# Optimization experiments

Hardware: AMD Instinct MI355X
Metric: run time of the kernel (lower is better)

## Reference

```python
import jax, jax.numpy as jnp
import numpy as np
from jax import lax

BN_EPS = 1e-5


def _spatial_gate(x, w, g, b, m, v):
    # x: [N, C, H, W]; ChannelPool -> [N, 2, H, W]; 7x7 conv -> [N,1,H,W]; BN (eval); sigmoid gate
    comp = jnp.stack([jnp.max(x, axis=1), jnp.mean(x, axis=1)], axis=1)
    o = lax.conv_general_dilated(comp, w, (1, 1), [(3, 3), (3, 3)],
                                 dimension_numbers=('NCHW', 'OIHW', 'NCHW'))
    o = (o - m[None, :, None, None]) * lax.rsqrt(v + BN_EPS)[None, :, None, None] \
        * g[None, :, None, None] + b[None, :, None, None]
    s = jax.nn.sigmoid(o)
    return x * s


def _eca_sort(x, w_eca):
    # global avg pool -> sort channels desc -> 1D conv over sorted seq -> sigmoid -> unsort -> gate
    y = jnp.mean(x, axis=(2, 3))               # [N, C]
    order = jnp.argsort(-y, axis=1)            # descending sort indices
    rank = jnp.argsort(order, axis=1)          # inverse permutation
    ys = jnp.take_along_axis(y, order, axis=1)  # sorted descending
    k = w_eca.shape[-1]
    p = k // 2
    o = lax.conv_general_dilated(ys[:, None, :], w_eca, (1,), [(p, p)],
                                 dimension_numbers=('NCH', 'OIH', 'NCH'))[:, 0, :]
    sig = jax.nn.sigmoid(o)
    yr = jnp.take_along_axis(sig, rank, axis=1)  # reorder back per original index_select(rank)
    return x * yr[:, :, None, None]


def setup_inputs() -> dict:
    key = jax.random.key(0)
    ks = jax.random.split(key, 6)
    N, C, H, W = 32, 256, 56, 56
    inp = {
        'x': jax.random.normal(ks[0], (N, C, H, W), dtype=jnp.float32),
        'weight': jax.random.normal(ks[1], (1,), dtype=jnp.float32),
        'w_h': jax.random.normal(ks[2], (1, 2, 7, 7), dtype=jnp.float32) * 0.1,
        'g_h': jnp.ones((1,), jnp.float32), 'b_h': jnp.zeros((1,), jnp.float32),
        'm_h': jnp.zeros((1,), jnp.float32), 'v_h': jnp.ones((1,), jnp.float32),
        'w_w': jax.random.normal(ks[3], (1, 2, 7, 7), dtype=jnp.float32) * 0.1,
        'g_w': jnp.ones((1,), jnp.float32), 'b_w': jnp.zeros((1,), jnp.float32),
        'm_w': jnp.zeros((1,), jnp.float32), 'v_w': jnp.ones((1,), jnp.float32),
        'w_s': jax.random.normal(ks[4], (1, 2, 7, 7), dtype=jnp.float32) * 0.1,
        'g_s': jnp.ones((1,), jnp.float32), 'b_s': jnp.zeros((1,), jnp.float32),
        'm_s': jnp.zeros((1,), jnp.float32), 'v_s': jnp.ones((1,), jnp.float32),
        'w_eca': jax.random.normal(ks[5], (1, 1, 5), dtype=jnp.float32) * 0.3,
    }
    return inp


def reference(x, weight, w_h, g_h, b_h, m_h, v_h, w_w, g_w, b_w, m_w, v_w,
              w_s, g_s, b_s, m_s, v_s, w_eca):
    # branch 1: gate over H-as-channel (permute 0,2,1,3)
    xh = jnp.transpose(x, (0, 2, 1, 3))
    x11 = jnp.transpose(_spatial_gate(xh, w_h, g_h, b_h, m_h, v_h), (0, 2, 1, 3))
    # branch 2: gate over W-as-channel (permute 0,3,2,1)
    xw = jnp.transpose(x, (0, 3, 2, 1))
    x21 = jnp.transpose(_spatial_gate(xw, w_w, g_w, b_w, m_w, v_w), (0, 3, 2, 1))
    # branch 3: eca with sort/unsort
    x31 = _eca_sort(x, w_eca)
    # branch 4: plain spatial gate
    xo = _spatial_gate(x, w_s, g_s, b_s, m_s, v_s)
    return 0.23779 * xo + 0.24695 * x11 + 0.24365 * x21 + 0.27173 * x31
```

## Files before the change

kernel.cpp:

```cpp
#include <hip/hip_runtime.h>
#include <math.h>

#define N_ 32
#define C_ 256
#define H_ 56
#define W_ 56
#define HW_ (H_*W_)
#define HW4_ (HW_/4)
#define CHW_ (C_*HW_)
#define NHW_ (N_*HW_)
#define NHW4_ (NHW_/4)
#define NCW_ (N_*C_*W_)
#define NHC_ (N_*H_*C_)
#define BN_EPS_ 1e-5f

#define TLD 60
#define PPB 8
#define NB_PL 1024

#define SM_BUF(i) ((i) * 3360)
#define SM_YS 6720
#define SM_TOT (6720 + 8)

#define F4MAX(a,b) do { (a).x=fmaxf((a).x,(b).x); (a).y=fmaxf((a).y,(b).y); \
                        (a).z=fmaxf((a).z,(b).z); (a).w=fmaxf((a).w,(b).w); } while(0)
#define F4ADD(a,b) do { (a).x+=(b).x; (a).y+=(b).y; (a).z+=(b).z; (a).w+=(b).w; } while(0)

__global__ __launch_bounds__(256, 4) void pools_k(
        const float* __restrict__ x,
        float* __restrict__ maxH, float* __restrict__ meanH,
        float* __restrict__ maxWt, float* __restrict__ meanWt,
        float* __restrict__ pmx, float* __restrict__ psm,
        float* __restrict__ y) {
    __shared__ float smem[SM_TOT];
    int b = blockIdx.x;
    int tid = threadIdx.x;
    const float4* x4 = (const float4*)x;
    int pb0 = b * PPB;
    int row0 = tid / 14,          col0 = (tid % 14) * 4;
    int row1 = (tid + 256) / 14,  col1 = ((tid + 256) % 14) * 4;
    int row2 = (tid + 512) / 14,  col2 = ((tid + 512) % 14) * 4;
    int row3 = (tid + 768) / 14,  col3 = ((tid + 768) % 14) * 4;
    int wq = tid >> 2, q4 = tid & 3;
    bool act = tid < 224;
    int wvid = tid >> 6;
    float4 a0, a1, a2, a3, b0_, b1_, b2_, b3_;
    float4 amx0, amx1, amx2, amx3, asm0, asm1, asm2, asm3;
    amx0 = amx1 = amx2 = amx3 = make_float4(-INFINITY, -INFINITY, -INFINITY, -INFINITY);
    asm0 = asm1 = asm2 = asm3 = make_float4(0.f, 0.f, 0.f, 0.f);

#define ISSUE(R0,R1,R2,R3, P) { size_t _ba = (size_t)(pb0 + (P)) * HW4_;          \
        R0 = x4[_ba + tid]; R1 = x4[_ba + 256 + tid]; R2 = x4[_ba + 512 + tid];   \
        if (tid < 16) R3 = x4[_ba + 768 + tid]; }
#define FOLD(R0,R1,R2,R3) { F4MAX(amx0,R0); F4ADD(asm0,R0);                       \
        F4MAX(amx1,R1); F4ADD(asm1,R1); F4MAX(amx2,R2); F4ADD(asm2,R2);           \
        if (tid < 16) { F4MAX(amx3,R3); F4ADD(asm3,R3); } }
#define STAGE(BUF, R0,R1,R2,R3) { float* _d = smem + (BUF);                       \
        *(float4*)&_d[row0*TLD+col0] = R0; *(float4*)&_d[row1*TLD+col1] = R1;     \
        *(float4*)&_d[row2*TLD+col2] = R2;                                        \
        if (tid < 16) *(float4*)&_d[row3*TLD+col3] = R3; }

    ISSUE(a0, a1, a2, a3, 0);
    FOLD(a0, a1, a2, a3);
    STAGE(SM_BUF(0), a0, a1, a2, a3);
    ISSUE(b0_, b1_, b2_, b3_, 1);
    __syncthreads();

    #pragma unroll
    for (int k = 0; k < PPB; ++k) {
        if (k + 2 < PPB) {
            if ((k & 1) == 0) { ISSUE(a0, a1, a2, a3, k + 2); }
            else              { ISSUE(b0_, b1_, b2_, b3_, k + 2); }
        }
        const float* cur = smem + SM_BUF(k & 1);
        int pb = pb0 + k;
        int n = pb >> 8, c = pb & 255;
        float cmx = -INFINITY, csm = 0.f, rmx = -INFINITY, rsm = 0.f;
        if (act) {
            const float* cb = &cur[(q4 * 14) * TLD + wq];
            #pragma unroll
            for (int hh = 0; hh < 14; ++hh) {
                float v = cb[hh * TLD];
                cmx = fmaxf(cmx, v); csm += v;
            }
            const float* rb = &cur[wq * TLD + q4 * 14];
            #pragma unroll
            for (int kk = 0; kk < 14; ++kk) {
                float v = rb[kk];
                rmx = fmaxf(rmx, v); rsm += v;
            }
        }
        cmx = fmaxf(cmx, __shfl_xor(cmx, 1)); csm += __shfl_xor(csm, 1);
        cmx = fmaxf(cmx, __shfl_xor(cmx, 2)); csm += __shfl_xor(csm, 2);
        rmx = fmaxf(rmx, __shfl_xor(rmx, 1)); rsm += __shfl_xor(rsm, 1);
        rmx = fmaxf(rmx, __shfl_xor(rmx, 2)); rsm += __shfl_xor(rsm, 2);
        if (act && q4 == 0) {
            int oH = (n * C_ + c) * W_ + wq;
            maxH[oH] = cmx; meanH[oH] = csm * (1.f / H_);
            int oW = (n * C_ + c) * H_ + wq;
            maxWt[oW] = rmx; meanWt[oW] = rsm * (1.f / W_);
        }
        float rs = (act && q4 == 0) ? rsm : 0.f;
        #pragma unroll
        for (int off = 32; off >= 1; off >>= 1) rs += __shfl_xor(rs, off);
        if ((tid & 63) == 0) smem[SM_YS + (k & 1) * 4 + wvid] = rs;
        if (k > 0 && tid == 0) {
            int s = ((k - 1) & 1) * 4;
            float t = smem[SM_YS + s] + smem[SM_YS + s + 1] +
                      smem[SM_YS + s + 2] + smem[SM_YS + s + 3];
            y[pb - 1] = t * (1.f / HW_);
        }
        if (k + 1 < PPB) {
            if ((k & 1) == 0) { FOLD(b0_, b1_, b2_, b3_);
                                STAGE(SM_BUF((k + 1) & 1), b0_, b1_, b2_, b3_); }
            else              { FOLD(a0, a1, a2, a3);
                                STAGE(SM_BUF((k + 1) & 1), a0, a1, a2, a3); }
        }
        __syncthreads();
    }
    if (tid == 0) {
        int s = ((PPB - 1) & 1) * 4;
        float t = smem[SM_YS + s] + smem[SM_YS + s + 1] +
                  smem[SM_YS + s + 2] + smem[SM_YS + s + 3];
        y[pb0 + PPB - 1] = t * (1.f / HW_);
    }
#undef ISSUE
#undef FOLD
#undef STAGE
    {
        float4* PM = (float4*)pmx + (size_t)b * HW4_;
        float4* PS = (float4*)psm + (size_t)b * HW4_;
        PM[tid] = amx0;        PS[tid] = asm0;
        PM[tid + 256] = amx1;  PS[tid + 256] = asm1;
        PM[tid + 512] = amx2;  PS[tid + 512] = asm2;
        if (tid < 16) { PM[tid + 768] = amx3; PS[tid + 768] = asm3; }
    }
}

__global__ __launch_bounds__(256, 4) void cpool_final_k(
        const float* __restrict__ pmx, const float* __restrict__ psm,
        float* __restrict__ maxC, float* __restrict__ meanC) {
    __shared__ float4 smx[4][64];
    __shared__ float4 ssm[4][64];
    int bb = blockIdx.x;
    int tid = threadIdx.x;
    int oi = tid & 63, g4 = tid >> 6;
    int t = bb * 64 + oi;
    int n = t / HW4_, hw4 = t - n * HW4_;
    const float4* PM = (const float4*)pmx + (size_t)(n * 32 + g4 * 8) * HW4_ + hw4;
    const float4* PS = (const float4*)psm + (size_t)(n * 32 + g4 * 8) * HW4_ + hw4;
    float4 mx = make_float4(-INFINITY, -INFINITY, -INFINITY, -INFINITY);
    float4 sm = make_float4(0.f, 0.f, 0.f, 0.f);
    #pragma unroll
    for (int g = 0; g < 8; ++g) {
        float4 v = PM[(size_t)g * HW4_];
        float4 s = PS[(size_t)g * HW4_];
        F4MAX(mx, v);
        F4ADD(sm, s);
    }
    smx[g4][oi] = mx;
    ssm[g4][oi] = sm;
    __syncthreads();
    if (tid < 64) {
        float4 m = smx[0][tid];
        #pragma unroll
        for (int j = 1; j < 4; ++j) F4MAX(m, smx[j][tid]);
        ((float4*)maxC)[bb * 64 + tid] = m;
    } else if (tid < 128) {
        int t2 = tid - 64;
        float4 s = ssm[0][t2];
        #pragma unroll
        for (int j = 1; j < 4; ++j) F4ADD(s, ssm[j][t2]);
        s.x *= (1.f / C_); s.y *= (1.f / C_); s.z *= (1.f / C_); s.w *= (1.f / C_);
        ((float4*)meanC)[bb * 64 + t2] = s;
    }
}

template <int R, int Cc, bool TR>
__device__ __forceinline__ void conv7_part(int t, const float* __restrict__ p0,
                                           const float* __restrict__ p1,
                                           const float* __restrict__ wt,
                                           float g, float bb, float m, float v,
                                           float* __restrict__ out) {
    const int per = R * Cc;
    int n = t / per;
    int r2 = t - n * per;
    int i = r2 / Cc, j = r2 - i * Cc;
    const float* b0 = p0 + (size_t)n * per;
    const float* b1 = p1 + (size_t)n * per;
    float acc = 0.f;
    #pragma unroll
    for (int ki = 0; ki < 7; ++ki) {
        int ii = i + ki - 3;
        if (ii < 0 || ii >= R) continue;
        #pragma unroll
        for (int kj = 0; kj < 7; ++kj) {
            int jj = j + kj - 3;
            if (jj < 0 || jj >= Cc) continue;
            int idx = ii * Cc + jj;
            int wi = TR ? (kj * 7 + ki) : (ki * 7 + kj);
            acc += b0[idx] * wt[wi] + b1[idx] * wt[49 + wi];
        }
    }
    float o = (acc - m) * rsqrtf(v + BN_EPS_) * g + bb;
    out[t] = 1.f / (1.f + expf(-o));
}

#define NB_SS (NHW_ / 256)
#define NB_SH (NCW_ / 256)
#define NB_SW (NHC_ / 256)

__global__ __launch_bounds__(256) void conv_eca_k(
        const float* __restrict__ maxC, const float* __restrict__ meanC,
        const float* __restrict__ maxH, const float* __restrict__ meanH,
        const float* __restrict__ maxWt, const float* __restrict__ meanWt,
        const float* __restrict__ w_s, const float* __restrict__ g_s,
        const float* __restrict__ b_s, const float* __restrict__ m_s,
        const float* __restrict__ v_s,
        const float* __restrict__ w_h, const float* __restrict__ g_h,
        const float* __restrict__ b_h, const float* __restrict__ m_h,
        const float* __restrict__ v_h,
        const float* __restrict__ w_w, const float* __restrict__ g_w,
        const float* __restrict__ b_w, const float* __restrict__ m_w,
        const float* __restrict__ v_w,
        const float* __restrict__ y, const float* __restrict__ w_eca,
        float* __restrict__ s_s, float* __restrict__ s_h, float* __restrict__ s_wt,
        float* __restrict__ gate) {
    __shared__ float sv[C_];
    __shared__ int si[C_];
    int b = blockIdx.x;
    int tid = threadIdx.x;
    if (b < NB_SS) {
        conv7_part<H_, W_, false>(b * 256 + tid, maxC, meanC, w_s, g_s[0], b_s[0],
                                  m_s[0], v_s[0], s_s);
    } else if (b < NB_SS + NB_SH) {
        conv7_part<C_, W_, false>((b - NB_SS) * 256 + tid, maxH, meanH, w_h, g_h[0],
                                  b_h[0], m_h[0], v_h[0], s_h);
    } else if (b < NB_SS + NB_SH + NB_SW) {
        conv7_part<C_, H_, true>((b - NB_SS - NB_SH) * 256 + tid, maxWt, meanWt, w_w,
                                 g_w[0], b_w[0], m_w[0], v_w[0], s_wt);
    } else {
        int n = b - (NB_SS + NB_SH + NB_SW);
        sv[tid] = y[n * C_ + tid];
        si[tid] = tid;
        __syncthreads();
        for (int k = 2; k <= C_; k <<= 1) {
            for (int j = k >> 1; j > 0; j >>= 1) {
                int ixj = tid ^ j;
                if (ixj > tid) {
                    float v1 = sv[tid], v2 = sv[ixj];
                    int i1 = si[tid], i2 = si[ixj];
                    bool before = (v1 > v2) || (v1 == v2 && i1 < i2);
                    bool dir = ((tid & k) == 0);
                    if (dir ? !before : before) {
                        sv[tid] = v2; sv[ixj] = v1;
                        si[tid] = i2; si[ixj] = i1;
                    }
                }
                __syncthreads();
            }
        }
        float o = 0.f;
        #pragma unroll
        for (int j = 0; j < 5; ++j) {
            int p = tid + j - 2;
            if (p >= 0 && p < C_) o += sv[p] * w_eca[j];
        }
        gate[n * C_ + si[tid]] = 1.f / (1.f + expf(-o));
    }
}

__global__ __launch_bounds__(256) void apply_k(
        const float* __restrict__ x, const float* __restrict__ s_s,
        const float* __restrict__ s_h, const float* __restrict__ s_wt,
        const float* __restrict__ gate, float* __restrict__ out) {
    int t0 = blockIdx.x * 512 + threadIdx.x;
    #pragma unroll
    for (int r = 0; r < 2; ++r) {
        int t = t0 + r * 256;
        int f = t * 4;
        int n = f / CHW_;
        int rem = f - n * CHW_;
        int c = rem / HW_;
        int hw = rem - c * HW_;
        int h = hw / W_;
        int w = hw - h * W_;
        float4 xv = ((const float4*)x)[t];
        float4 s4 = *(const float4*)(s_s + (size_t)n * HW_ + hw);
        float4 h4 = *(const float4*)(s_h + ((size_t)n * C_ + c) * W_ + w);
        float sw = s_wt[((size_t)n * C_ + c) * H_ + h];
        float ge = gate[n * C_ + c];
        float base = 0.24365f * sw + 0.27173f * ge;
        float4 o;
        o.x = xv.x * (0.23779f * s4.x + 0.24695f * h4.x + base);
        o.y = xv.y * (0.23779f * s4.y + 0.24695f * h4.y + base);
        o.z = xv.z * (0.23779f * s4.z + 0.24695f * h4.z + base);
        o.w = xv.w * (0.23779f * s4.w + 0.24695f * h4.w + base);
        ((float4*)out)[t] = o;
    }
}

extern "C" void kernel_launch(void* const* d_in, const int* in_sizes, int n_in,
                              void* d_out, int out_size, void* d_ws, size_t ws_size,
                              hipStream_t stream) {
    const float* x     = (const float*)d_in[0];
    const float* w_h   = (const float*)d_in[2];
    const float* g_h   = (const float*)d_in[3];
    const float* b_h   = (const float*)d_in[4];
    const float* m_h   = (const float*)d_in[5];
    const float* v_h   = (const float*)d_in[6];
    const float* w_w   = (const float*)d_in[7];
    const float* g_w   = (const float*)d_in[8];
    const float* b_w   = (const float*)d_in[9];
    const float* m_w   = (const float*)d_in[10];
    const float* v_w   = (const float*)d_in[11];
    const float* w_s   = (const float*)d_in[12];
    const float* g_s   = (const float*)d_in[13];
    const float* b_s   = (const float*)d_in[14];
    const float* m_s   = (const float*)d_in[15];
    const float* v_s   = (const float*)d_in[16];
    const float* w_eca = (const float*)d_in[17];
    float* out = (float*)d_out;

    float* ws    = (float*)d_ws;
    float* maxC  = ws;
    float* meanC = maxC  + NHW_;
    float* maxH  = meanC + NHW_;
    float* meanH = maxH  + NCW_;
    float* maxWt = meanH + NCW_;
    float* meanWt= maxWt + NHC_;
    float* s_s   = meanWt+ NHC_;
    float* s_h   = s_s   + NHW_;
    float* s_wt  = s_h   + NCW_;
    float* yv    = s_wt  + NHC_;
    float* gate  = yv    + N_ * C_;
    float* pmx   = gate  + N_ * C_;
    float* psm   = pmx   + (size_t)NB_PL * HW_;

    pools_k<<<NB_PL, 256, 0, stream>>>(x, maxH, meanH, maxWt, meanWt, pmx, psm, yv);

    cpool_final_k<<<NHW4_ / 64, 256, 0, stream>>>(pmx, psm, maxC, meanC);

    int conv_blocks = NB_SS + NB_SH + NB_SW + N_;
    conv_eca_k<<<conv_blocks, 256, 0, stream>>>(maxC, meanC, maxH, meanH, maxWt, meanWt,
                                                w_s, g_s, b_s, m_s, v_s,
                                                w_h, g_h, b_h, m_h, v_h,
                                                w_w, g_w, b_w, m_w, v_w,
                                                yv, w_eca, s_s, s_h, s_wt, gate);

    apply_k<<<(N_ * CHW_ / 4) / 512, 256, 0, stream>>>(x, s_s, s_h, s_wt, gate, out);
}
```

Measured before the change: 112.1 us.

## Restructure pooling kernel to one wavefront per block with register-held planes

Rewrites pools_k so each 64-thread block (one wavefront) processes 8 channel planes. Each lane holds a whole column strip of the plane in registers and double-buffers two planes, in place of a 256-thread block staging tiles through shared memory with block-wide barriers. Column reductions happen in registers, and row reductions go through a small shared scratch within the wavefront, which removes __syncthreads. The trade-off is much higher register pressure (about 56 float4 registers per lane), lower occupancy, and 8 idle lanes out of 64 on the loads.

```diff
diff --git a/kernel.cpp b/kernel.cpp
--- a/kernel.cpp
+++ b/kernel.cpp
@@ -14,126 +14,108 @@
 #define NHC_ (N_*H_*C_)
 #define BN_EPS_ 1e-5f
 
-#define TLD 60
-#define PPB 8
+#define PPW 8
 #define NB_PL 1024
-
-#define SM_BUF(i) ((i) * 3360)
-#define SM_YS 6720
-#define SM_TOT (6720 + 8)
 
 #define F4MAX(a,b) do { (a).x=fmaxf((a).x,(b).x); (a).y=fmaxf((a).y,(b).y); \
                         (a).z=fmaxf((a).z,(b).z); (a).w=fmaxf((a).w,(b).w); } while(0)
 #define F4ADD(a,b) do { (a).x+=(b).x; (a).y+=(b).y; (a).z+=(b).z; (a).w+=(b).w; } while(0)
 
-__global__ __launch_bounds__(256, 4) void pools_k(
+__global__ __launch_bounds__(64) void pools_k(
         const float* __restrict__ x,
         float* __restrict__ maxH, float* __restrict__ meanH,
         float* __restrict__ maxWt, float* __restrict__ meanWt,
         float* __restrict__ pmx, float* __restrict__ psm,
         float* __restrict__ y) {
-    __shared__ float smem[SM_TOT];
-    int b = blockIdx.x;
-    int tid = threadIdx.x;
+    __shared__ float2 rowscr[56 * 15];
+    __shared__ float4 colmx[56];
+    __shared__ float4 colsm[56];
+    const int wid = blockIdx.x;
+    const int lane = threadIdx.x;
+    const int n = wid >> 5;
+    const int pb0 = wid * PPW;
     const float4* x4 = (const float4*)x;
-    int pb0 = b * PPB;
-    int row0 = tid / 14,          col0 = (tid % 14) * 4;
-    int row1 = (tid + 256) / 14,  col1 = ((tid + 256) % 14) * 4;
-    int row2 = (tid + 512) / 14,  col2 = ((tid + 512) % 14) * 4;
-    int row3 = (tid + 768) / 14,  col3 = ((tid + 768) % 14) * 4;
-    int wq = tid >> 2, q4 = tid & 3;
-    bool act = tid < 224;
-    int wvid = tid >> 6;
-    float4 a0, a1, a2, a3, b0_, b1_, b2_, b3_;
-    float4 amx0, amx1, amx2, amx3, asm0, asm1, asm2, asm3;
-    amx0 = amx1 = amx2 = amx3 = make_float4(-INFINITY, -INFINITY, -INFINITY, -INFINITY);
-    asm0 = asm1 = asm2 = asm3 = make_float4(0.f, 0.f, 0.f, 0.f);
-
-#define ISSUE(R0,R1,R2,R3, P) { size_t _ba = (size_t)(pb0 + (P)) * HW4_;          \
-        R0 = x4[_ba + tid]; R1 = x4[_ba + 256 + tid]; R2 = x4[_ba + 512 + tid];   \
-        if (tid < 16) R3 = x4[_ba + 768 + tid]; }
-#define FOLD(R0,R1,R2,R3) { F4MAX(amx0,R0); F4ADD(asm0,R0);                       \
-        F4MAX(amx1,R1); F4ADD(asm1,R1); F4MAX(amx2,R2); F4ADD(asm2,R2);           \
-        if (tid < 16) { F4MAX(amx3,R3); F4ADD(asm3,R3); } }
-#define STAGE(BUF, R0,R1,R2,R3) { float* _d = smem + (BUF);                       \
-        *(float4*)&_d[row0*TLD+col0] = R0; *(float4*)&_d[row1*TLD+col1] = R1;     \
-        *(float4*)&_d[row2*TLD+col2] = R2;                                        \
-        if (tid < 16) *(float4*)&_d[row3*TLD+col3] = R3; }
-
-    ISSUE(a0, a1, a2, a3, 0);
-    FOLD(a0, a1, a2, a3);
-    STAGE(SM_BUF(0), a0, a1, a2, a3);
-    ISSUE(b0_, b1_, b2_, b3_, 1);
-    __syncthreads();
-
-    #pragma unroll
-    for (int k = 0; k < PPB; ++k) {
-        if (k + 2 < PPB) {
-            if ((k & 1) == 0) { ISSUE(a0, a1, a2, a3, k + 2); }
-            else              { ISSUE(b0_, b1_, b2_, b3_, k + 2); }
+    const int lc = (lane < 56) ? lane : 55;
+    const int g = lane / 14;
+    const int q = lane - g * 14;
+
+    float4 A[14], B[14];
+    float4 amx[14], asum[14];
+    #pragma unroll
+    for (int t = 0; t < 14; ++t) {
+        amx[t] = make_float4(-INFINITY, -INFINITY, -INFINITY, -INFINITY);
+        asum[t] = make_float4(0.f, 0.f, 0.f, 0.f);
+    }
+
+#define ISSUE(S, P) do { size_t _ba = (size_t)(pb0 + (P)) * HW4_;                  \
+        _Pragma("unroll")                                                          \
+        for (int _t = 0; _t < 14; ++_t) S[_t] = x4[_ba + 56 * _t + lc]; } while(0)
+
+#define PLANE(S, K) do {                                                           \
+        const int _pb = pb0 + (K);                                                 \
+        const int _c = _pb & 255;                                                  \
+        float4 cmx = S[0], csm = S[0];                                             \
+        _Pragma("unroll")                                                          \
+        for (int t = 1; t < 14; ++t) { F4MAX(cmx, S[t]); F4ADD(csm, S[t]); }       \
+        _Pragma("unroll")                                                          \
+        for (int t = 0; t < 14; ++t) { F4MAX(amx[t], S[t]); F4ADD(asum[t], S[t]); }\
+        if (lane < 56) {                                                           \
+            _Pragma("unroll")                                                      \
+            for (int t = 0; t < 14; ++t) {                                         \
+                float hm = fmaxf(fmaxf(S[t].x, S[t].y), fmaxf(S[t].z, S[t].w));    \
+                float hs = S[t].x + S[t].y + S[t].z + S[t].w;                      \
+                rowscr[(4 * t + g) * 15 + q] = make_float2(hm, hs);                \
+            }                                                                      \
+            colmx[g * 14 + q] = cmx;                                               \
+            colsm[g * 14 + q] = csm;                                               \
+        }                                                                          \
+        if ((K) + 2 < PPW) ISSUE(S, (K) + 2);         \
+        if (lane < 56) {                               \
+            float rmx = -INFINITY, rsm = 0.f;                                      \
+            _Pragma("unroll")                                                      \
+            for (int j = 0; j < 14; ++j) {                                         \
+                float2 p = rowscr[lane * 15 + j];                                  \
+                rmx = fmaxf(rmx, p.x); rsm += p.y;                                 \
+            }                                                                      \
+            int o = (n * C_ + _c) * H_ + lane;          \
+            maxWt[o] = rmx; meanWt[o] = rsm * (1.f / W_);                          \
+        }                                                                          \
+        float ysum = 0.f;                                                          \
+        if (lane < 14) {                        \
+            float4 gm = colmx[lane], gs = colsm[lane];                             \
+            _Pragma("unroll")                                                      \
+            for (int j = 1; j < 4; ++j) {                                          \
+                F4MAX(gm, colmx[j * 14 + lane]);                                   \
+                F4ADD(gs, colsm[j * 14 + lane]);                                   \
+            }                                                                      \
+            ((float4*)maxH)[(n * C_ + _c) * 14 + lane] = gm;                       \
+            float4 mh = make_float4(gs.x * (1.f / H_), gs.y * (1.f / H_),          \
+                                    gs.z * (1.f / H_), gs.w * (1.f / H_));         \
+            ((float4*)meanH)[(n * C_ + _c) * 14 + lane] = mh;                      \
+            ysum = gs.x + gs.y + gs.z + gs.w;                                      \
+        }                                                                          \
+        ysum += __shfl_down(ysum, 8); ysum += __shfl_down(ysum, 4);                \
+        ysum += __shfl_down(ysum, 2); ysum += __shfl_down(ysum, 1);                \
+        if (lane == 0) y[_pb] = ysum * (1.f / HW_);                                \
+    } while(0)
+
+    ISSUE(A, 0);
+    ISSUE(B, 1);
+    #pragma unroll
+    for (int k2 = 0; k2 < PPW / 2; ++k2) {
+        PLANE(A, 2 * k2);
+        PLANE(B, 2 * k2 + 1);
+    }
+#undef ISSUE
+#undef PLANE
+    if (lane < 56) {
+        float4* PM = (float4*)pmx + (size_t)wid * HW4_;
+        float4* PS = (float4*)psm + (size_t)wid * HW4_;
+        #pragma unroll
+        for (int t = 0; t < 14; ++t) {
+            PM[56 * t + lane] = amx[t];
+            PS[56 * t + lane] = asum[t];
         }
-        const float* cur = smem + SM_BUF(k & 1);
-        int pb = pb0 + k;
-        int n = pb >> 8, c = pb & 255;
-        float cmx = -INFINITY, csm = 0.f, rmx = -INFINITY, rsm = 0.f;
-        if (act) {
-            const float* cb = &cur[(q4 * 14) * TLD + wq];
-            #pragma unroll
-            for (int hh = 0; hh < 14; ++hh) {
-                float v = cb[hh * TLD];
-                cmx = fmaxf(cmx, v); csm += v;
-            }
-            const float* rb = &cur[wq * TLD + q4 * 14];
-            #pragma unroll
-            for (int kk = 0; kk < 14; ++kk) {
-                float v = rb[kk];
-                rmx = fmaxf(rmx, v); rsm += v;
-            }
-        }
-        cmx = fmaxf(cmx, __shfl_xor(cmx, 1)); csm += __shfl_xor(csm, 1);
-        cmx = fmaxf(cmx, __shfl_xor(cmx, 2)); csm += __shfl_xor(csm, 2);
-        rmx = fmaxf(rmx, __shfl_xor(rmx, 1)); rsm += __shfl_xor(rsm, 1);
-        rmx = fmaxf(rmx, __shfl_xor(rmx, 2)); rsm += __shfl_xor(rsm, 2);
-        if (act && q4 == 0) {
-            int oH = (n * C_ + c) * W_ + wq;
-            maxH[oH] = cmx; meanH[oH] = csm * (1.f / H_);
-            int oW = (n * C_ + c) * H_ + wq;
-            maxWt[oW] = rmx; meanWt[oW] = rsm * (1.f / W_);
-        }
-        float rs = (act && q4 == 0) ? rsm : 0.f;
-        #pragma unroll
-        for (int off = 32; off >= 1; off >>= 1) rs += __shfl_xor(rs, off);
-        if ((tid & 63) == 0) smem[SM_YS + (k & 1) * 4 + wvid] = rs;
-        if (k > 0 && tid == 0) {
-            int s = ((k - 1) & 1) * 4;
-            float t = smem[SM_YS + s] + smem[SM_YS + s + 1] +
-                      smem[SM_YS + s + 2] + smem[SM_YS + s + 3];
-            y[pb - 1] = t * (1.f / HW_);
-        }
-        if (k + 1 < PPB) {
-            if ((k & 1) == 0) { FOLD(b0_, b1_, b2_, b3_);
-                                STAGE(SM_BUF((k + 1) & 1), b0_, b1_, b2_, b3_); }
-            else              { FOLD(a0, a1, a2, a3);
-                                STAGE(SM_BUF((k + 1) & 1), a0, a1, a2, a3); }
-        }
-        __syncthreads();
-    }
-    if (tid == 0) {
-        int s = ((PPB - 1) & 1) * 4;
-        float t = smem[SM_YS + s] + smem[SM_YS + s + 1] +
-                  smem[SM_YS + s + 2] + smem[SM_YS + s + 3];
-        y[pb0 + PPB - 1] = t * (1.f / HW_);
-    }
-#undef ISSUE
-#undef FOLD
-#undef STAGE
-    {
-        float4* PM = (float4*)pmx + (size_t)b * HW4_;
-        float4* PS = (float4*)psm + (size_t)b * HW4_;
-        PM[tid] = amx0;        PS[tid] = asm0;
-        PM[tid + 256] = amx1;  PS[tid + 256] = asm1;
-        PM[tid + 512] = amx2;  PS[tid + 512] = asm2;
-        if (tid < 16) { PM[tid + 768] = amx3; PS[tid + 768] = asm3; }
     }
 }
 
@@ -337,7 +319,7 @@
     float* pmx   = gate  + N_ * C_;
     float* psm   = pmx   + (size_t)NB_PL * HW_;
 
-    pools_k<<<NB_PL, 256, 0, stream>>>(x, maxH, meanH, maxWt, meanWt, pmx, psm, yv);
+    pools_k<<<NB_PL, 64, 0, stream>>>(x, maxH, meanH, maxWt, meanWt, pmx, psm, yv);
 
     cpool_final_k<<<NHW4_ / 64, 256, 0, stream>>>(pmx, psm, maxC, meanC);
 
```

New measurement: 94.65 us. 15.6% less time.

## Stream input planes into LDS with direct global_load_lds DMA

Applied to the files above, without the earlier changes.

The pools kernel no longer loads each plane into registers and then writes it to a padded LDS tile. It now uses the global_load_lds builtin to copy 16-byte chunks straight from global memory into an unpadded double-buffered LDS plane. The channel max/sum accumulation reads from LDS instead of from the held registers, and prefetch depth drops from two planes to one. The aim is to cut VGPR pressure and the register-to-LDS store traffic. The risks are LDS bank conflicts from the unpadded 56-float row stride on column reads, and less latency hiding with the shallower prefetch.

```diff
diff --git a/kernel.cpp b/kernel.cpp
--- a/kernel.cpp
+++ b/kernel.cpp
@@ -14,17 +14,15 @@
 #define NHC_ (N_*H_*C_)
 #define BN_EPS_ 1e-5f
 
-#define TLD 60
 #define PPB 8
 #define NB_PL 1024
-
-#define SM_BUF(i) ((i) * 3360)
-#define SM_YS 6720
-#define SM_TOT (6720 + 8)
 
 #define F4MAX(a,b) do { (a).x=fmaxf((a).x,(b).x); (a).y=fmaxf((a).y,(b).y); \
                         (a).z=fmaxf((a).z,(b).z); (a).w=fmaxf((a).w,(b).w); } while(0)
 #define F4ADD(a,b) do { (a).x+=(b).x; (a).y+=(b).y; (a).z+=(b).z; (a).w+=(b).w; } while(0)
+
+typedef __attribute__((address_space(1))) const unsigned int GAS;
+typedef __attribute__((address_space(3))) unsigned int LAS;
 
 __global__ __launch_bounds__(256, 4) void pools_k(
         const float* __restrict__ x,
@@ -32,101 +30,111 @@
         float* __restrict__ maxWt, float* __restrict__ meanWt,
         float* __restrict__ pmx, float* __restrict__ psm,
         float* __restrict__ y) {
-    __shared__ float smem[SM_TOT];
-    int b = blockIdx.x;
-    int tid = threadIdx.x;
+    __shared__ float buf[2][HW_];
+    __shared__ float ys[8];
+    const int b = blockIdx.x;
+    const int tid = threadIdx.x;
+    const int wave = tid >> 6;
+    const int lane = tid & 63;
+    const int n = b >> 5;
+    const int pb0 = b * PPB;
     const float4* x4 = (const float4*)x;
-    int pb0 = b * PPB;
-    int row0 = tid / 14,          col0 = (tid % 14) * 4;
-    int row1 = (tid + 256) / 14,  col1 = ((tid + 256) % 14) * 4;
-    int row2 = (tid + 512) / 14,  col2 = ((tid + 512) % 14) * 4;
-    int row3 = (tid + 768) / 14,  col3 = ((tid + 768) % 14) * 4;
-    int wq = tid >> 2, q4 = tid & 3;
-    bool act = tid < 224;
-    int wvid = tid >> 6;
-    float4 a0, a1, a2, a3, b0_, b1_, b2_, b3_;
+
     float4 amx0, amx1, amx2, amx3, asm0, asm1, asm2, asm3;
     amx0 = amx1 = amx2 = amx3 = make_float4(-INFINITY, -INFINITY, -INFINITY, -INFINITY);
     asm0 = asm1 = asm2 = asm3 = make_float4(0.f, 0.f, 0.f, 0.f);
 
-#define ISSUE(R0,R1,R2,R3, P) { size_t _ba = (size_t)(pb0 + (P)) * HW4_;          \
-        R0 = x4[_ba + tid]; R1 = x4[_ba + 256 + tid]; R2 = x4[_ba + 512 + tid];   \
-        if (tid < 16) R3 = x4[_ba + 768 + tid]; }
-#define FOLD(R0,R1,R2,R3) { F4MAX(amx0,R0); F4ADD(asm0,R0);                       \
-        F4MAX(amx1,R1); F4ADD(asm1,R1); F4MAX(amx2,R2); F4ADD(asm2,R2);           \
-        if (tid < 16) { F4MAX(amx3,R3); F4ADD(asm3,R3); } }
-#define STAGE(BUF, R0,R1,R2,R3) { float* _d = smem + (BUF);                       \
-        *(float4*)&_d[row0*TLD+col0] = R0; *(float4*)&_d[row1*TLD+col1] = R1;     \
-        *(float4*)&_d[row2*TLD+col2] = R2;                                        \
-        if (tid < 16) *(float4*)&_d[row3*TLD+col3] = R3; }
-
-    ISSUE(a0, a1, a2, a3, 0);
-    FOLD(a0, a1, a2, a3);
-    STAGE(SM_BUF(0), a0, a1, a2, a3);
-    ISSUE(b0_, b1_, b2_, b3_, 1);
+#define ISSUE(P, PAR) do {                                                         \
+        size_t _gb = (size_t)(pb0 + (P)) * HW4_;                                   \
+        _Pragma("unroll")                                                          \
+        for (int _ch = 0; _ch < 3; ++_ch) {                                        \
+            int _c = wave * 3 + _ch;                                               \
+            __builtin_amdgcn_global_load_lds((GAS*)(x4 + _gb + _c * 64 + lane),    \
+                                             (LAS*)&buf[PAR][_c * 256], 16, 0, 0); \
+        }                                                                          \
+        if (tid < 16)                                                              \
+            __builtin_amdgcn_global_load_lds((GAS*)(x4 + _gb + 768 + lane),        \
+                                             (LAS*)&buf[PAR][3072], 16, 0, 0);     \
+    } while (0)
+
+    ISSUE(0, 0);
     __syncthreads();
 
     #pragma unroll
     for (int k = 0; k < PPB; ++k) {
-        if (k + 2 < PPB) {
-            if ((k & 1) == 0) { ISSUE(a0, a1, a2, a3, k + 2); }
-            else              { ISSUE(b0_, b1_, b2_, b3_, k + 2); }
-        }
-        const float* cur = smem + SM_BUF(k & 1);
-        int pb = pb0 + k;
-        int n = pb >> 8, c = pb & 255;
-        float cmx = -INFINITY, csm = 0.f, rmx = -INFINITY, rsm = 0.f;
-        if (act) {
-            const float* cb = &cur[(q4 * 14) * TLD + wq];
+        const int par = k & 1;
+        if (k + 1 < PPB) ISSUE(k + 1, par ^ 1);
+
+        const float* tile = buf[par];
+        const float4* tile4 = (const float4*)tile;
+        const int pb = pb0 + k;
+        const int c = pb & 255;
+
+        {
+            float4 v0 = tile4[tid];
+            float4 v1 = tile4[tid + 256];
+            float4 v2 = tile4[tid + 512];
+            F4MAX(amx0, v0); F4ADD(asm0, v0);
+            F4MAX(amx1, v1); F4ADD(asm1, v1);
+            F4MAX(amx2, v2); F4ADD(asm2, v2);
+            if (tid < 16) {
+                float4 v3 = tile4[tid + 768];
+                F4MAX(amx3, v3); F4ADD(asm3, v3);
+            }
+        }
+        float csm_full = 0.f;
+        if (tid < 224) {
+            int w = tid >> 2, hq = tid & 3;
+            float cmx = -INFINITY, csm = 0.f;
             #pragma unroll
             for (int hh = 0; hh < 14; ++hh) {
-                float v = cb[hh * TLD];
+                float v = tile[(hq * 14 + hh) * W_ + w];
                 cmx = fmaxf(cmx, v); csm += v;
             }
-            const float* rb = &cur[wq * TLD + q4 * 14];
+            cmx = fmaxf(cmx, __shfl_xor(cmx, 1)); csm += __shfl_xor(csm, 1);
+            cmx = fmaxf(cmx, __shfl_xor(cmx, 2)); csm += __shfl_xor(csm, 2);
+            if (hq == 0) {
+                int o = (n * C_ + c) * W_ + w;
+                maxH[o] = cmx;
+                meanH[o] = csm * (1.f / H_);
+                csm_full = csm;
+            }
+        }
+        if (tid < 224) {
+            int h = tid >> 2, kq = tid & 3;
+            float rmx = -INFINITY, rsm = 0.f;
             #pragma unroll
-            for (int kk = 0; kk < 14; ++kk) {
-                float v = rb[kk];
+            for (int j = 0; j < 14; ++j) {
+                float v = tile[h * W_ + kq * 14 + j];
                 rmx = fmaxf(rmx, v); rsm += v;
             }
-        }
-        cmx = fmaxf(cmx, __shfl_xor(cmx, 1)); csm += __shfl_xor(csm, 1);
-        cmx = fmaxf(cmx, __shfl_xor(cmx, 2)); csm += __shfl_xor(csm, 2);
-        rmx = fmaxf(rmx, __shfl_xor(rmx, 1)); rsm += __shfl_xor(rsm, 1);
-        rmx = fmaxf(rmx, __shfl_xor(rmx, 2)); rsm += __shfl_xor(rsm, 2);
-        if (act && q4 == 0) {
-            int oH = (n * C_ + c) * W_ + wq;
-            maxH[oH] = cmx; meanH[oH] = csm * (1.f / H_);
-            int oW = (n * C_ + c) * H_ + wq;
-            maxWt[oW] = rmx; meanWt[oW] = rsm * (1.f / W_);
-        }
-        float rs = (act && q4 == 0) ? rsm : 0.f;
-        #pragma unroll
-        for (int off = 32; off >= 1; off >>= 1) rs += __shfl_xor(rs, off);
-        if ((tid & 63) == 0) smem[SM_YS + (k & 1) * 4 + wvid] = rs;
-        if (k > 0 && tid == 0) {
-            int s = ((k - 1) & 1) * 4;
-            float t = smem[SM_YS + s] + smem[SM_YS + s + 1] +
-                      smem[SM_YS + s + 2] + smem[SM_YS + s + 3];
-            y[pb - 1] = t * (1.f / HW_);
-        }
-        if (k + 1 < PPB) {
-            if ((k & 1) == 0) { FOLD(b0_, b1_, b2_, b3_);
-                                STAGE(SM_BUF((k + 1) & 1), b0_, b1_, b2_, b3_); }
-            else              { FOLD(a0, a1, a2, a3);
-                                STAGE(SM_BUF((k + 1) & 1), a0, a1, a2, a3); }
+            rmx = fmaxf(rmx, __shfl_xor(rmx, 1)); rsm += __shfl_xor(rsm, 1);
+            rmx = fmaxf(rmx, __shfl_xor(rmx, 2)); rsm += __shfl_xor(rsm, 2);
+            if (kq == 0) {
+                int o = (n * C_ + c) * H_ + h;
+                maxWt[o] = rmx;
+                meanWt[o] = rsm * (1.f / W_);
+            }
+        }
+        {
+            float yp = csm_full;
+            #pragma unroll
+            for (int off = 32; off >= 1; off >>= 1) yp += __shfl_xor(yp, off);
+            if (lane == 0) ys[par * 4 + wave] = yp;
+            if (k > 0 && tid == 0) {
+                int s = (par ^ 1) * 4;
+                float t = ys[s] + ys[s + 1] + ys[s + 2] + ys[s + 3];
+                y[pb - 1] = t * (1.f / HW_);
+            }
         }
         __syncthreads();
     }
     if (tid == 0) {
         int s = ((PPB - 1) & 1) * 4;
-        float t = smem[SM_YS + s] + smem[SM_YS + s + 1] +
-                  smem[SM_YS + s + 2] + smem[SM_YS + s + 3];
+        float t = ys[s] + ys[s + 1] + ys[s + 2] + ys[s + 3];
         y[pb0 + PPB - 1] = t * (1.f / HW_);
     }
 #undef ISSUE
-#undef FOLD
-#undef STAGE
     {
         float4* PM = (float4*)pmx + (size_t)b * HW4_;
         float4* PS = (float4*)psm + (size_t)b * HW4_;
```

Result: faster. 96.78 us (-13.7%).
